# Performance work log

Measured on AMD Instinct MI355X. Metric: run time of the kernel, lower is better.

Reference implementation:

```python
import jax, jax.numpy as jnp
import numpy as np

BN_EPS = 1e-5


def _bn_train(x, gamma, beta):
    # torch BatchNorm1d in training mode: normalize with batch mean and
    # biased batch variance.
    mu = jnp.mean(x, axis=0)
    var = jnp.var(x, axis=0)
    return (x - mu) * jax.lax.rsqrt(var + BN_EPS) * gamma + beta


def setup_inputs() -> dict:
    key = jax.random.key(0)
    ks = jax.random.split(key, 12)
    N, F_D, F_C, E, VOCAB, H = 16384, 26, 10, 16, 200000, 400
    D_IN = (F_D + F_C) * E  # 576
    return {
        "Xi_dense": jax.random.normal(ks[0], (N, F_D, 1), jnp.float32),
        "Xv": jax.random.uniform(ks[1], (N, F_D + F_C), jnp.float32),
        "Wd": jax.random.normal(ks[2], (F_D, E), jnp.float32) * 0.1,
        "bd": jax.random.normal(ks[3], (F_D, E), jnp.float32) * 0.1,
        "tables": jax.random.normal(ks[4], (F_C, VOCAB, E), jnp.float32) * 0.1,
        "W1": jax.random.normal(ks[5], (H, D_IN), jnp.float32) * 0.05,
        "b1": jax.random.normal(ks[6], (H,), jnp.float32) * 0.05,
        "g1": jnp.ones((H,), jnp.float32),
        "be1": jnp.zeros((H,), jnp.float32),
        "W2": jax.random.normal(ks[7], (H, H), jnp.float32) * 0.05,
        "b2": jax.random.normal(ks[8], (H,), jnp.float32) * 0.05,
        "g2": jnp.ones((H,), jnp.float32),
        "be2": jnp.zeros((H,), jnp.float32),
        "bias_vec": jax.random.normal(ks[9], (N,), jnp.float32),
        "Xi_cat": jax.random.randint(ks[10], (N, F_C, 1), 0, VOCAB, jnp.int32),
    }


def reference(Xi_dense, Xv, Wd, bd, tables, W1, b1, g1, be1,
              W2, b2, g2, be2, bias_vec, Xi_cat):
    N = Xi_dense.shape[0]
    # dense fields: per-field Linear(1, E) -> x * W + b, shape (N, 26, E)
    dense_emb = Xi_dense * Wd[None] + bd[None]  # (N,26,1)*(1,26,E) broadcast
    # categorical fields: per-field embedding lookup, shape (N, 10, E)
    cat_emb = jax.vmap(lambda tbl, idx: tbl[idx], in_axes=(0, 1), out_axes=1)(
        tables, Xi_cat[:, :, 0])
    # scale each field embedding by its Xv value
    all_emb = jnp.concatenate([dense_emb, cat_emb], axis=1) * Xv[:, :, None]  # (N,36,E)

    # fm first order: concat of all scaled field embeddings
    fm_first = all_emb.reshape(N, -1)  # (N, 576)
    # fm second order: 0.5 * ((sum)^2 - sum of squares)
    s = jnp.sum(all_emb, axis=1)                       # (N, E)
    fm_second = 0.5 * (s * s - jnp.sum(all_emb * all_emb, axis=1))  # (N, E)

    # deep part: Linear -> BatchNorm (train-mode stats) per hidden layer;
    # dropout p=0 -> identity.
    deep = fm_first
    deep = _bn_train(deep @ W1.T + b1, g1, be1)
    deep = _bn_train(deep @ W2.T + b2, g2, be2)

    total = (jnp.sum(fm_first, axis=1) + jnp.sum(fm_second, axis=1)
             + jnp.sum(deep, axis=1) + bias_vec)
    return total
```

## Files before the change

### kernel.cpp

```cpp
#include <hip/hip_runtime.h>

#define BN_EPS 1e-5f

typedef unsigned short u16;
typedef __attribute__((ext_vector_type(8))) short bf16x8;
typedef __attribute__((ext_vector_type(4))) float f32x4;

__device__ __forceinline__ u16 f2bf(float x) {
  union { float f; unsigned int u; } v; v.f = x;
  unsigned int r = v.u + 0x7fffu + ((v.u >> 16) & 1u);
  return (u16)(r >> 16);
}
__device__ __forceinline__ float bf2f(u16 h) {
  union { unsigned int u; float f; } v; v.u = ((unsigned int)h) << 16;
  return v.f;
}

__device__ __forceinline__ float wave_reduce_sum(float v) {
#pragma unroll
  for (int off = 1; off < 64; off <<= 1) v += __shfl_xor(v, off, 64);
  return v;
}

__device__ __forceinline__ void gload_lds16(const void* g, void* l) {
  __builtin_amdgcn_global_load_lds(
      (const __attribute__((address_space(1))) void*)g,
      (__attribute__((address_space(3))) void*)l, 16, 0, 0);
}

#define NBE 4096
__global__ __launch_bounds__(256) void embed_prep(
    const float* __restrict__ Xi_dense, const float* __restrict__ Xv,
    const float* __restrict__ Wd, const float* __restrict__ bd,
    const float* __restrict__ tables, const int* __restrict__ Xi_cat,
    const float* __restrict__ bias_vec, const float* __restrict__ W1,
    u16* __restrict__ fm_first, float* __restrict__ partial,
    u16* __restrict__ W1h) {
  const int t = threadIdx.x;
  if (blockIdx.x >= NBE) {
    const int base = (blockIdx.x - NBE) * 4096;
#pragma unroll
    for (int e = 0; e < 16; ++e) {
      const int idx = base + e * 256 + t;
      const int r = idx / 576;
      const int j = idx - r * 576;
      W1h[idx] = (r < 400) ? f2bf(W1[r * 576 + j]) : (u16)0;
    }
    return;
  }
  const int lane = t & 63;
  const int n = blockIdx.x * 4 + (t >> 6);

  const float* xv = Xv + n * 36;
  float sum_all = 0.f, s_e = 0.f, q_e = 0.f;

#pragma unroll
  for (int k = 0; k < 9; ++k) {
    const int idx = lane + 64 * k;
    const int f = idx >> 4;
    const int e = idx & 15;
    float val;
    if (f < 26) {
      val = Xi_dense[n * 26 + f] * Wd[f * 16 + e] + bd[f * 16 + e];
    } else {
      const int fc = f - 26;
      const int row = Xi_cat[n * 10 + fc];
      val = tables[(size_t)fc * 200000 * 16 + (size_t)row * 16 + e];
    }
    val *= xv[f];
    fm_first[(size_t)n * 576 + idx] = f2bf(val);
    sum_all += val;
    s_e += val;
    q_e += val * val;
  }

  float s_tot = s_e;
  s_tot += __shfl_xor(s_tot, 16, 64);
  s_tot += __shfl_xor(s_tot, 32, 64);
  float q_tot = q_e;
  q_tot += __shfl_xor(q_tot, 16, 64);
  q_tot += __shfl_xor(q_tot, 32, 64);

  const float fm2 = 0.5f * (s_tot * s_tot - q_tot);
  const float red1 = wave_reduce_sum(sum_all);
  const float red2 = wave_reduce_sum(fm2) * 0.25f;
  if (lane == 0) partial[n] = red1 + red2 + bias_vec[n];
}

__global__ __launch_bounds__(256) void gemm_bf16(
    const u16* __restrict__ A, int lda,
    const u16* __restrict__ W, int ldw,
    const float* __restrict__ bias, int nbias,
    u16* __restrict__ Y, int ldc, int Ncap,
    float* __restrict__ pS, float* __restrict__ pQ, int K) {
  __shared__ u16 As[128 * 32];
  __shared__ u16 Bs[128 * 32];
  __shared__ float rS[2][4][2][16];
  __shared__ float rQ[2][4][2][16];

  const int t = threadIdx.x;
  const int bm = blockIdx.x * 128;
  const int bn = blockIdx.y * 128;
  const int wid = t >> 6, lane = t & 63;
  const int wr = wid >> 1, wc = wid & 1;
  const int lr = lane & 15, lk = (lane >> 4) * 8;
  const int sr = lane >> 2;
  const int sk = (lane & 3) * 8;

  f32x4 acc[4][4] = {};

  for (int kt = 0; kt < K; kt += 32) {
#pragma unroll
    for (int i = 0; i < 2; ++i) {
      const int c = wid * 2 + i;
      gload_lds16(&A[(size_t)(bm + c * 16 + sr) * lda + kt + sk],
                  &As[c * 512]);
      gload_lds16(&W[(size_t)(bn + c * 16 + sr) * ldw + kt + sk],
                  &Bs[c * 512]);
    }
    __syncthreads();

    bf16x8 af[4], bfv[4];
#pragma unroll
    for (int mf = 0; mf < 4; ++mf)
      af[mf] = *(const bf16x8*)&As[(wr * 64 + mf * 16 + lr) * 32 + lk];
#pragma unroll
    for (int nf = 0; nf < 4; ++nf)
      bfv[nf] = *(const bf16x8*)&Bs[(wc * 64 + nf * 16 + lr) * 32 + lk];
#pragma unroll
    for (int mf = 0; mf < 4; ++mf)
#pragma unroll
      for (int nf = 0; nf < 4; ++nf)
        acc[mf][nf] = __builtin_amdgcn_mfma_f32_16x16x32_bf16(
            af[mf], bfv[nf], acc[mf][nf], 0, 0, 0);
    __syncthreads();
  }

  const int l4 = (lane >> 4) * 4;
#pragma unroll
  for (int nf = 0; nf < 4; ++nf) {
    const int col = bn + wc * 64 + nf * 16 + lr;
    const float bb = (col < nbias) ? bias[col] : 0.f;
    float s = 0.f, q = 0.f;
#pragma unroll
    for (int mf = 0; mf < 4; ++mf) {
#pragma unroll
      for (int r = 0; r < 4; ++r) {
        const int row = bm + wr * 64 + mf * 16 + l4 + r;
        const float v = acc[mf][nf][r] + bb;
        s += v;
        q += v * v;
        if (col < Ncap) Y[(size_t)row * ldc + col] = f2bf(v);
      }
    }
    s += __shfl_xor(s, 16, 64);
    s += __shfl_xor(s, 32, 64);
    q += __shfl_xor(q, 16, 64);
    q += __shfl_xor(q, 32, 64);
    if (lane < 16) {
      rS[wc][nf][wr][lr] = s;
      rQ[wc][nf][wr][lr] = q;
    }
  }
  __syncthreads();
  if (t < 128) {
    const int wcc = t >> 6, nff = (t >> 4) & 3, c = t & 15;
    pS[(size_t)(bn + t) * gridDim.x + blockIdx.x] =
        rS[wcc][nff][0][c] + rS[wcc][nff][1][c];
    pQ[(size_t)(bn + t) * gridDim.x + blockIdx.x] =
        rQ[wcc][nff][0][c] + rQ[wcc][nff][1][c];
  }
}

__global__ __launch_bounds__(256) void bn_ac(
    const float* __restrict__ pS, const float* __restrict__ pQ,
    const float* __restrict__ g, const float* __restrict__ be,
    float* __restrict__ a, float* __restrict__ c) {
  const int wid = threadIdx.x >> 6, lane = threadIdx.x & 63;
  const int col = blockIdx.x * 4 + wid;
  float S = pS[(size_t)col * 128 + lane] + pS[(size_t)col * 128 + 64 + lane];
  float Q = pQ[(size_t)col * 128 + lane] + pQ[(size_t)col * 128 + 64 + lane];
#pragma unroll
  for (int off = 1; off < 64; off <<= 1) {
    S += __shfl_xor(S, off, 64);
    Q += __shfl_xor(Q, off, 64);
  }
  if (lane == 0) {
    const float mu = S * (1.f / 16384.f);
    const float var = Q * (1.f / 16384.f) - mu * mu;
    const float aa = g[col] * rsqrtf(var + BN_EPS);
    a[col] = aa;
    c[col] = be[col] - mu * aa;
  }
}

__global__ __launch_bounds__(256) void prep2(
    const float* __restrict__ a1, const float* __restrict__ c1,
    const float* __restrict__ W2, const float* __restrict__ b2,
    u16* __restrict__ W2p, float* __restrict__ b2p) {
  const int t = threadIdx.x;
  const int lane = t & 63;
  const int row = blockIdx.x * 4 + (t >> 6);
  const ushort4 z4 = {0, 0, 0, 0};
  if (row >= 400) {
    const int j1 = lane * 4;
    *(ushort4*)&W2p[(size_t)row * 416 + j1] = z4;
    const int j2 = 256 + lane * 4;
    if (j2 < 416) *(ushort4*)&W2p[(size_t)row * 416 + j2] = z4;
    if (lane == 0) b2p[row] = 0.f;
    return;
  }
  float dot = 0.f;
  {
    const int j = lane * 4;
    const float4 w = *(const float4*)&W2[(size_t)row * 400 + j];
    const float4 la = *(const float4*)&a1[j];
    const float4 lc = *(const float4*)&c1[j];
    ushort4 o = {f2bf(w.x * la.x), f2bf(w.y * la.y), f2bf(w.z * la.z),
                 f2bf(w.w * la.w)};
    *(ushort4*)&W2p[(size_t)row * 416 + j] = o;
    dot += w.x * lc.x + w.y * lc.y + w.z * lc.z + w.w * lc.w;
  }
  {
    const int j = 256 + lane * 4;
    if (j < 400) {
      const float4 w = *(const float4*)&W2[(size_t)row * 400 + j];
      const float4 la = *(const float4*)&a1[j];
      const float4 lc = *(const float4*)&c1[j];
      ushort4 o = {f2bf(w.x * la.x), f2bf(w.y * la.y), f2bf(w.z * la.z),
                   f2bf(w.w * la.w)};
      *(ushort4*)&W2p[(size_t)row * 416 + j] = o;
      dot += w.x * lc.x + w.y * lc.y + w.z * lc.z + w.w * lc.w;
    } else if (j < 416) {
      *(ushort4*)&W2p[(size_t)row * 416 + j] = z4;
    }
  }
  dot = wave_reduce_sum(dot);
  if (lane == 0) b2p[row] = b2[row] + dot;
}

__global__ __launch_bounds__(256) void final_kernel(
    const u16* __restrict__ Y2, const float* __restrict__ a2,
    const float* __restrict__ c2, const float* __restrict__ partial,
    float* __restrict__ out) {
  const int t = threadIdx.x;
  const int lane = t & 63;
  const int wid = t >> 6;
  const int j0 = lane * 8;
  float ar[8], cr[8];
  if (j0 < 400) {
    const float4 a0 = *(const float4*)&a2[j0];
    const float4 a1v = *(const float4*)&a2[j0 + 4];
    const float4 c0 = *(const float4*)&c2[j0];
    const float4 c1v = *(const float4*)&c2[j0 + 4];
    ar[0] = a0.x; ar[1] = a0.y; ar[2] = a0.z; ar[3] = a0.w;
    ar[4] = a1v.x; ar[5] = a1v.y; ar[6] = a1v.z; ar[7] = a1v.w;
    cr[0] = c0.x; cr[1] = c0.y; cr[2] = c0.z; cr[3] = c0.w;
    cr[4] = c1v.x; cr[5] = c1v.y; cr[6] = c1v.z; cr[7] = c1v.w;
  } else {
#pragma unroll
    for (int k = 0; k < 8; ++k) { ar[k] = 0.f; cr[k] = 0.f; }
  }
#pragma unroll
  for (int r = 0; r < 4; ++r) {
    const int n = blockIdx.x * 16 + wid * 4 + r;
    float acc = 0.f;
    if (j0 < 400) {
      const bf16x8 y = *(const bf16x8*)&Y2[(size_t)n * 400 + j0];
#pragma unroll
      for (int k = 0; k < 8; ++k)
        acc += fmaf(ar[k], bf2f((u16)y[k]), cr[k]);
    }
    acc = wave_reduce_sum(acc);
    if (lane == 0) out[n] = partial[n] + acc;
  }
}

extern "C" void kernel_launch(void* const* d_in, const int* in_sizes, int n_in,
                              void* d_out, int out_size, void* d_ws,
                              size_t ws_size, hipStream_t stream) {
  const float* Xi_dense = (const float*)d_in[0];
  const float* Xv = (const float*)d_in[1];
  const float* Wd = (const float*)d_in[2];
  const float* bd = (const float*)d_in[3];
  const float* tables = (const float*)d_in[4];
  const float* W1 = (const float*)d_in[5];
  const float* b1 = (const float*)d_in[6];
  const float* g1 = (const float*)d_in[7];
  const float* be1 = (const float*)d_in[8];
  const float* W2 = (const float*)d_in[9];
  const float* b2 = (const float*)d_in[10];
  const float* g2 = (const float*)d_in[11];
  const float* be2 = (const float*)d_in[12];
  const float* bias_vec = (const float*)d_in[13];
  const int* Xi_cat = (const int*)d_in[14];

  constexpr int N = 16384;
  constexpr int DIN = 576;
  constexpr int H = 400;
  constexpr int KP = 416;
  constexpr int WPAD = 512;
  constexpr int MB = 128;

  u16* fm_first = (u16*)d_ws;
  u16* Y1h = fm_first + (size_t)N * DIN;
  u16* Y2h = Y1h + (size_t)N * KP;
  u16* W1h = Y2h + (size_t)N * H;
  u16* W2p = W1h + (size_t)WPAD * DIN;
  float* fptr = (float*)(W2p + (size_t)WPAD * KP);
  float* partial = fptr;
  float* pS = partial + N;
  float* pQ = pS + WPAD * MB;
  float* a1 = pQ + WPAD * MB;
  float* c1 = a1 + WPAD;
  float* a2 = c1 + WPAD;
  float* c2 = a2 + WPAD;
  float* b2p = c2 + WPAD;

  embed_prep<<<NBE + 72, 256, 0, stream>>>(Xi_dense, Xv, Wd, bd, tables,
                                           Xi_cat, bias_vec, W1, fm_first,
                                           partial, W1h);

  dim3 gg(MB, 4);
  gemm_bf16<<<gg, 256, 0, stream>>>(fm_first, DIN, W1h, DIN, b1, H,
                                    Y1h, KP, KP, pS, pQ, DIN);

  bn_ac<<<100, 256, 0, stream>>>(pS, pQ, g1, be1, a1, c1);
  prep2<<<MB, 256, 0, stream>>>(a1, c1, W2, b2, W2p, b2p);

  gemm_bf16<<<gg, 256, 0, stream>>>(Y1h, KP, W2p, KP, b2p, H,
                                    Y2h, H, H, pS, pQ, KP);

  bn_ac<<<100, 256, 0, stream>>>(pS, pQ, g2, be2, a2, c2);

  final_kernel<<<N / 16, 256, 0, stream>>>(Y2h, a2, c2, partial,
                                           (float*)d_out);
}
```

Measured before the change: 71.13 us.

## Shrink GEMM M-tile to 64, trim padded N-tile, and swizzle block order

The GEMM moves from 128x128 to 64x128 tiles and launches 1024 blocks on a 1D grid instead of 512. The last N-tile, which covers columns 384-511 with only 16 of them useful for H=400, now uses a 2-fragment variant in which half the waves stay idle and skip the padded MFMA work. Block indices are remapped with a stride-8 swizzle to change how tiles are assigned across CUs/XCDs. This raises occupancy and trims wasted padded compute, at the cost of more A-tile reloads and more partial BN sums that bn_ac has to reduce.

```diff
diff --git a/kernel.cpp b/kernel.cpp
--- a/kernel.cpp
+++ b/kernel.cpp
@@ -87,99 +87,125 @@
   if (lane == 0) partial[n] = red1 + red2 + bias_vec[n];
 }
 
+template <int NFR>
+__device__ __forceinline__ void gemm_body(
+    const u16* __restrict__ A, int lda, const u16* __restrict__ W, int ldw,
+    const float* __restrict__ bias, int nbias, u16* __restrict__ Y, int ldc,
+    int Ncap, float* __restrict__ pS, float* __restrict__ pQ, int K, int nxb,
+    int bx, int by, u16* As, u16* Bs, float (&rS)[2][4][2][16],
+    float (&rQ)[2][4][2][16]) {
+  const int t = threadIdx.x;
+  const int bm = bx * 64;
+  const int bn = by * 128;
+  const int wid = t >> 6, lane = t & 63;
+  const int wr = wid >> 1, wc = wid & 1;
+  const int lr = lane & 15, lk = (lane >> 4) * 8;
+  const int sr = lane >> 2;
+  const int sk = (lane & 3) * 8;
+  const bool active = (NFR == 4) || (wc == 0);
+
+  f32x4 acc[2][NFR] = {};
+
+  for (int kt = 0; kt < K; kt += 32) {
+    gload_lds16(&A[(size_t)(bm + wid * 16 + sr) * lda + kt + sk],
+                &As[wid * 512]);
+#pragma unroll
+    for (int i = 0; i < 2; ++i) {
+      const int c = wid * 2 + i;
+      if (NFR == 4 || c < 2)
+        gload_lds16(&W[(size_t)(bn + c * 16 + sr) * ldw + kt + sk],
+                    &Bs[c * 512]);
+    }
+    __syncthreads();
+
+    if (active) {
+      bf16x8 af[2], bfv[NFR];
+#pragma unroll
+      for (int mf = 0; mf < 2; ++mf)
+        af[mf] = *(const bf16x8*)&As[(wr * 32 + mf * 16 + lr) * 32 + lk];
+#pragma unroll
+      for (int nf = 0; nf < NFR; ++nf)
+        bfv[nf] = *(const bf16x8*)&Bs[(wc * 64 + nf * 16 + lr) * 32 + lk];
+#pragma unroll
+      for (int mf = 0; mf < 2; ++mf)
+#pragma unroll
+        for (int nf = 0; nf < NFR; ++nf)
+          acc[mf][nf] = __builtin_amdgcn_mfma_f32_16x16x32_bf16(
+              af[mf], bfv[nf], acc[mf][nf], 0, 0, 0);
+    }
+    __syncthreads();
+  }
+
+  const int l4 = (lane >> 4) * 4;
+  if (active) {
+#pragma unroll
+    for (int nf = 0; nf < NFR; ++nf) {
+      const int col = bn + wc * 64 + nf * 16 + lr;
+      const float bb = (col < nbias) ? bias[col] : 0.f;
+      float s = 0.f, q = 0.f;
+#pragma unroll
+      for (int mf = 0; mf < 2; ++mf) {
+#pragma unroll
+        for (int r = 0; r < 4; ++r) {
+          const int row = bm + wr * 32 + mf * 16 + l4 + r;
+          const float v = acc[mf][nf][r] + bb;
+          s += v;
+          q += v * v;
+          if (col < Ncap) Y[(size_t)row * ldc + col] = f2bf(v);
+        }
+      }
+      s += __shfl_xor(s, 16, 64);
+      s += __shfl_xor(s, 32, 64);
+      q += __shfl_xor(q, 16, 64);
+      q += __shfl_xor(q, 32, 64);
+      if (lane < 16) {
+        rS[wc][nf][wr][lr] = s;
+        rQ[wc][nf][wr][lr] = q;
+      }
+    }
+  }
+  __syncthreads();
+  if (t < (NFR == 4 ? 128 : 32)) {
+    const int wcc = t >> 6, nff = (t >> 4) & 3, c = t & 15;
+    pS[(size_t)(bn + t) * nxb + bx] =
+        rS[wcc][nff][0][c] + rS[wcc][nff][1][c];
+    pQ[(size_t)(bn + t) * nxb + bx] =
+        rQ[wcc][nff][0][c] + rQ[wcc][nff][1][c];
+  }
+}
+
 __global__ __launch_bounds__(256) void gemm_bf16(
     const u16* __restrict__ A, int lda,
     const u16* __restrict__ W, int ldw,
     const float* __restrict__ bias, int nbias,
     u16* __restrict__ Y, int ldc, int Ncap,
-    float* __restrict__ pS, float* __restrict__ pQ, int K) {
-  __shared__ u16 As[128 * 32];
+    float* __restrict__ pS, float* __restrict__ pQ, int K, int nxb) {
+  __shared__ u16 As[64 * 32];
   __shared__ u16 Bs[128 * 32];
   __shared__ float rS[2][4][2][16];
   __shared__ float rQ[2][4][2][16];
-
-  const int t = threadIdx.x;
-  const int bm = blockIdx.x * 128;
-  const int bn = blockIdx.y * 128;
-  const int wid = t >> 6, lane = t & 63;
-  const int wr = wid >> 1, wc = wid & 1;
-  const int lr = lane & 15, lk = (lane >> 4) * 8;
-  const int sr = lane >> 2;
-  const int sk = (lane & 3) * 8;
-
-  f32x4 acc[4][4] = {};
-
-  for (int kt = 0; kt < K; kt += 32) {
-#pragma unroll
-    for (int i = 0; i < 2; ++i) {
-      const int c = wid * 2 + i;
-      gload_lds16(&A[(size_t)(bm + c * 16 + sr) * lda + kt + sk],
-                  &As[c * 512]);
-      gload_lds16(&W[(size_t)(bn + c * 16 + sr) * ldw + kt + sk],
-                  &Bs[c * 512]);
-    }
-    __syncthreads();
-
-    bf16x8 af[4], bfv[4];
-#pragma unroll
-    for (int mf = 0; mf < 4; ++mf)
-      af[mf] = *(const bf16x8*)&As[(wr * 64 + mf * 16 + lr) * 32 + lk];
-#pragma unroll
-    for (int nf = 0; nf < 4; ++nf)
-      bfv[nf] = *(const bf16x8*)&Bs[(wc * 64 + nf * 16 + lr) * 32 + lk];
-#pragma unroll
-    for (int mf = 0; mf < 4; ++mf)
-#pragma unroll
-      for (int nf = 0; nf < 4; ++nf)
-        acc[mf][nf] = __builtin_amdgcn_mfma_f32_16x16x32_bf16(
-            af[mf], bfv[nf], acc[mf][nf], 0, 0, 0);
-    __syncthreads();
-  }
-
-  const int l4 = (lane >> 4) * 4;
-#pragma unroll
-  for (int nf = 0; nf < 4; ++nf) {
-    const int col = bn + wc * 64 + nf * 16 + lr;
-    const float bb = (col < nbias) ? bias[col] : 0.f;
-    float s = 0.f, q = 0.f;
-#pragma unroll
-    for (int mf = 0; mf < 4; ++mf) {
-#pragma unroll
-      for (int r = 0; r < 4; ++r) {
-        const int row = bm + wr * 64 + mf * 16 + l4 + r;
-        const float v = acc[mf][nf][r] + bb;
-        s += v;
-        q += v * v;
-        if (col < Ncap) Y[(size_t)row * ldc + col] = f2bf(v);
-      }
-    }
-    s += __shfl_xor(s, 16, 64);
-    s += __shfl_xor(s, 32, 64);
-    q += __shfl_xor(q, 16, 64);
-    q += __shfl_xor(q, 32, 64);
-    if (lane < 16) {
-      rS[wc][nf][wr][lr] = s;
-      rQ[wc][nf][wr][lr] = q;
-    }
-  }
-  __syncthreads();
-  if (t < 128) {
-    const int wcc = t >> 6, nff = (t >> 4) & 3, c = t & 15;
-    pS[(size_t)(bn + t) * gridDim.x + blockIdx.x] =
-        rS[wcc][nff][0][c] + rS[wcc][nff][1][c];
-    pQ[(size_t)(bn + t) * gridDim.x + blockIdx.x] =
-        rQ[wcc][nff][0][c] + rQ[wcc][nff][1][c];
-  }
+  const int bid = blockIdx.x;
+  const int l = (bid & 7) * (gridDim.x >> 3) + (bid >> 3);
+  const int bx = l >> 2, by = l & 3;
+  if (by < 3)
+    gemm_body<4>(A, lda, W, ldw, bias, nbias, Y, ldc, Ncap, pS, pQ, K, nxb,
+                 bx, by, As, Bs, rS, rQ);
+  else
+    gemm_body<2>(A, lda, W, ldw, bias, nbias, Y, ldc, Ncap, pS, pQ, K, nxb,
+                 bx, by, As, Bs, rS, rQ);
 }
 
 __global__ __launch_bounds__(256) void bn_ac(
     const float* __restrict__ pS, const float* __restrict__ pQ,
     const float* __restrict__ g, const float* __restrict__ be,
-    float* __restrict__ a, float* __restrict__ c) {
+    float* __restrict__ a, float* __restrict__ c, int nxb) {
   const int wid = threadIdx.x >> 6, lane = threadIdx.x & 63;
   const int col = blockIdx.x * 4 + wid;
-  float S = pS[(size_t)col * 128 + lane] + pS[(size_t)col * 128 + 64 + lane];
-  float Q = pQ[(size_t)col * 128 + lane] + pQ[(size_t)col * 128 + 64 + lane];
+  float S = 0.f, Q = 0.f;
+  for (int i = lane; i < nxb; i += 64) {
+    S += pS[(size_t)col * nxb + i];
+    Q += pQ[(size_t)col * nxb + i];
+  }
 #pragma unroll
   for (int off = 1; off < 64; off <<= 1) {
     S += __shfl_xor(S, off, 64);
@@ -300,7 +326,7 @@
   constexpr int H = 400;
   constexpr int KP = 416;
   constexpr int WPAD = 512;
-  constexpr int MB = 128;
+  constexpr int NXB = 256;
 
   u16* fm_first = (u16*)d_ws;
   u16* Y1h = fm_first + (size_t)N * DIN;
@@ -310,8 +336,8 @@
   float* fptr = (float*)(W2p + (size_t)WPAD * KP);
   float* partial = fptr;
   float* pS = partial + N;
-  float* pQ = pS + WPAD * MB;
-  float* a1 = pQ + WPAD * MB;
+  float* pQ = pS + WPAD * NXB;
+  float* a1 = pQ + WPAD * NXB;
   float* c1 = a1 + WPAD;
   float* a2 = c1 + WPAD;
   float* c2 = a2 + WPAD;
@@ -321,17 +347,16 @@
                                            Xi_cat, bias_vec, W1, fm_first,
                                            partial, W1h);
 
-  dim3 gg(MB, 4);
-  gemm_bf16<<<gg, 256, 0, stream>>>(fm_first, DIN, W1h, DIN, b1, H,
-                                    Y1h, KP, KP, pS, pQ, DIN);
-
-  bn_ac<<<100, 256, 0, stream>>>(pS, pQ, g1, be1, a1, c1);
-  prep2<<<MB, 256, 0, stream>>>(a1, c1, W2, b2, W2p, b2p);
-
-  gemm_bf16<<<gg, 256, 0, stream>>>(Y1h, KP, W2p, KP, b2p, H,
-                                    Y2h, H, H, pS, pQ, KP);
-
-  bn_ac<<<100, 256, 0, stream>>>(pS, pQ, g2, be2, a2, c2);
+  gemm_bf16<<<NXB * 4, 256, 0, stream>>>(fm_first, DIN, W1h, DIN, b1, H,
+                                         Y1h, KP, KP, pS, pQ, DIN, NXB);
+
+  bn_ac<<<100, 256, 0, stream>>>(pS, pQ, g1, be1, a1, c1, NXB);
+  prep2<<<128, 256, 0, stream>>>(a1, c1, W2, b2, W2p, b2p);
+
+  gemm_bf16<<<NXB * 4, 256, 0, stream>>>(Y1h, KP, W2p, KP, b2p, H,
+                                         Y2h, H, H, pS, pQ, KP, NXB);
+
+  bn_ac<<<100, 256, 0, stream>>>(pS, pQ, g2, be2, a2, c2, NXB);
 
   final_kernel<<<N / 16, 256, 0, stream>>>(Y2h, a2, c2, partial,
                                            (float*)d_out);
```

Result: faster. 67.88 us (-4.6%).

## Keep full weight panel in LDS and stream A from global into registers

Applied to the files above, without the earlier changes.

Replaces the 128x128 LDS-tiled GEMM with a templated 256x64-tile kernel. It loads the block's whole 64-column weight panel (padded) into LDS once. Each wave then streams its 64 A rows straight from global memory into registers, prefetching two k-steps ahead, so the per-k-step barriers go away. A swizzled 1D grid of 448 blocks and MFMA priority hints are added, and the BN partial-stat reduction is adapted to 64 row-blocks. This trades large LDS use and uncoalesced direct A loads for removing synchronization and improving B reuse.

```diff
diff --git a/kernel.cpp b/kernel.cpp
--- a/kernel.cpp
+++ b/kernel.cpp
@@ -20,12 +20,6 @@
 #pragma unroll
   for (int off = 1; off < 64; off <<= 1) v += __shfl_xor(v, off, 64);
   return v;
-}
-
-__device__ __forceinline__ void gload_lds16(const void* g, void* l) {
-  __builtin_amdgcn_global_load_lds(
-      (const __attribute__((address_space(1))) void*)g,
-      (__attribute__((address_space(3))) void*)l, 16, 0, 0);
 }
 
 #define NBE 4096
@@ -87,66 +81,91 @@
   if (lane == 0) partial[n] = red1 + red2 + bias_vec[n];
 }
 
-__global__ __launch_bounds__(256) void gemm_bf16(
-    const u16* __restrict__ A, int lda,
-    const u16* __restrict__ W, int ldw,
+template <int K>
+__global__ __launch_bounds__(256) void gemm_bres(
+    const u16* __restrict__ A,
+    const u16* __restrict__ W,
     const float* __restrict__ bias, int nbias,
     u16* __restrict__ Y, int ldc, int Ncap,
-    float* __restrict__ pS, float* __restrict__ pQ, int K) {
-  __shared__ u16 As[128 * 32];
-  __shared__ u16 Bs[128 * 32];
-  __shared__ float rS[2][4][2][16];
-  __shared__ float rQ[2][4][2][16];
+    float* __restrict__ pS, float* __restrict__ pQ) {
+  constexpr int NI = K / 32;
+  constexpr int PADK = K + 8;
+  constexpr int CPR = K / 8;
+  __shared__ u16 Bs[64 * PADK];
+  __shared__ float rS[4][64];
+  __shared__ float rQ[4][64];
 
   const int t = threadIdx.x;
-  const int bm = blockIdx.x * 128;
-  const int bn = blockIdx.y * 128;
+  const int bid = blockIdx.x;
+  const int l = (bid & 7) * 56 + (bid >> 3);
+  const int bx = l / 7;
+  const int by = l - bx * 7;
+  const int bm = bx * 256, bn = by * 64;
+
+  for (int chunk = t; chunk < 64 * CPR; chunk += 256) {
+    const int r = chunk / CPR;
+    const int cc = (chunk - r * CPR) * 8;
+    *(bf16x8*)&Bs[r * PADK + cc] =
+        *(const bf16x8*)&W[(size_t)(bn + r) * K + cc];
+  }
+  __syncthreads();
+
   const int wid = t >> 6, lane = t & 63;
-  const int wr = wid >> 1, wc = wid & 1;
   const int lr = lane & 15, lk = (lane >> 4) * 8;
-  const int sr = lane >> 2;
-  const int sk = (lane & 3) * 8;
+  const int rowb = bm + wid * 64;
+
+  const u16* Ap = A + (size_t)(rowb + lr) * K + lk;
 
   f32x4 acc[4][4] = {};
-
-  for (int kt = 0; kt < K; kt += 32) {
-#pragma unroll
-    for (int i = 0; i < 2; ++i) {
-      const int c = wid * 2 + i;
-      gload_lds16(&A[(size_t)(bm + c * 16 + sr) * lda + kt + sk],
-                  &As[c * 512]);
-      gload_lds16(&W[(size_t)(bn + c * 16 + sr) * ldw + kt + sk],
-                  &Bs[c * 512]);
-    }
-    __syncthreads();
-
-    bf16x8 af[4], bfv[4];
-#pragma unroll
-    for (int mf = 0; mf < 4; ++mf)
-      af[mf] = *(const bf16x8*)&As[(wr * 64 + mf * 16 + lr) * 32 + lk];
+  bf16x8 afA[4], afB[4];
+#pragma unroll
+  for (int mf = 0; mf < 4; ++mf) {
+    afA[mf] = *(const bf16x8*)&Ap[(size_t)mf * 16 * K];
+    afB[mf] = *(const bf16x8*)&Ap[(size_t)mf * 16 * K + 32];
+  }
+
+#pragma unroll
+  for (int i = 0; i < NI; ++i) {
+    const int kt = i * 32;
+    bf16x8 bv[4];
 #pragma unroll
     for (int nf = 0; nf < 4; ++nf)
-      bfv[nf] = *(const bf16x8*)&Bs[(wc * 64 + nf * 16 + lr) * 32 + lk];
+      bv[nf] = *(const bf16x8*)&Bs[(nf * 16 + lr) * PADK + kt + lk];
+    bf16x8 afN[4];
+    if (i + 2 < NI) {
+#pragma unroll
+      for (int mf = 0; mf < 4; ++mf)
+        afN[mf] = *(const bf16x8*)&Ap[(size_t)mf * 16 * K + kt + 64];
+    } else {
+#pragma unroll
+      for (int mf = 0; mf < 4; ++mf) afN[mf] = afB[mf];
+    }
+    __builtin_amdgcn_s_setprio(1);
 #pragma unroll
     for (int mf = 0; mf < 4; ++mf)
 #pragma unroll
       for (int nf = 0; nf < 4; ++nf)
         acc[mf][nf] = __builtin_amdgcn_mfma_f32_16x16x32_bf16(
-            af[mf], bfv[nf], acc[mf][nf], 0, 0, 0);
-    __syncthreads();
+            afA[mf], bv[nf], acc[mf][nf], 0, 0, 0);
+    __builtin_amdgcn_s_setprio(0);
+#pragma unroll
+    for (int mf = 0; mf < 4; ++mf) {
+      afA[mf] = afB[mf];
+      afB[mf] = afN[mf];
+    }
   }
 
   const int l4 = (lane >> 4) * 4;
 #pragma unroll
   for (int nf = 0; nf < 4; ++nf) {
-    const int col = bn + wc * 64 + nf * 16 + lr;
+    const int col = bn + nf * 16 + lr;
     const float bb = (col < nbias) ? bias[col] : 0.f;
     float s = 0.f, q = 0.f;
 #pragma unroll
     for (int mf = 0; mf < 4; ++mf) {
 #pragma unroll
       for (int r = 0; r < 4; ++r) {
-        const int row = bm + wr * 64 + mf * 16 + l4 + r;
+        const int row = rowb + mf * 16 + l4 + r;
         const float v = acc[mf][nf][r] + bb;
         s += v;
         q += v * v;
@@ -158,28 +177,30 @@
     q += __shfl_xor(q, 16, 64);
     q += __shfl_xor(q, 32, 64);
     if (lane < 16) {
-      rS[wc][nf][wr][lr] = s;
-      rQ[wc][nf][wr][lr] = q;
+      rS[wid][nf * 16 + lr] = s;
+      rQ[wid][nf * 16 + lr] = q;
     }
   }
   __syncthreads();
-  if (t < 128) {
-    const int wcc = t >> 6, nff = (t >> 4) & 3, c = t & 15;
-    pS[(size_t)(bn + t) * gridDim.x + blockIdx.x] =
-        rS[wcc][nff][0][c] + rS[wcc][nff][1][c];
-    pQ[(size_t)(bn + t) * gridDim.x + blockIdx.x] =
-        rQ[wcc][nff][0][c] + rQ[wcc][nff][1][c];
+  if (t < 64) {
+    const float S = rS[0][t] + rS[1][t] + rS[2][t] + rS[3][t];
+    const float Q = rQ[0][t] + rQ[1][t] + rQ[2][t] + rQ[3][t];
+    pS[(size_t)(bn + t) * 64 + bx] = S;
+    pQ[(size_t)(bn + t) * 64 + bx] = Q;
   }
 }
 
 __global__ __launch_bounds__(256) void bn_ac(
     const float* __restrict__ pS, const float* __restrict__ pQ,
     const float* __restrict__ g, const float* __restrict__ be,
-    float* __restrict__ a, float* __restrict__ c) {
+    float* __restrict__ a, float* __restrict__ c, int nxb) {
   const int wid = threadIdx.x >> 6, lane = threadIdx.x & 63;
   const int col = blockIdx.x * 4 + wid;
-  float S = pS[(size_t)col * 128 + lane] + pS[(size_t)col * 128 + 64 + lane];
-  float Q = pQ[(size_t)col * 128 + lane] + pQ[(size_t)col * 128 + 64 + lane];
+  float S = 0.f, Q = 0.f;
+  for (int i = lane; i < nxb; i += 64) {
+    S += pS[(size_t)col * nxb + i];
+    Q += pQ[(size_t)col * nxb + i];
+  }
 #pragma unroll
   for (int off = 1; off < 64; off <<= 1) {
     S += __shfl_xor(S, off, 64);
@@ -300,7 +321,7 @@
   constexpr int H = 400;
   constexpr int KP = 416;
   constexpr int WPAD = 512;
-  constexpr int MB = 128;
+  constexpr int NXB = 64;
 
   u16* fm_first = (u16*)d_ws;
   u16* Y1h = fm_first + (size_t)N * DIN;
@@ -310,8 +331,8 @@
   float* fptr = (float*)(W2p + (size_t)WPAD * KP);
   float* partial = fptr;
   float* pS = partial + N;
-  float* pQ = pS + WPAD * MB;
-  float* a1 = pQ + WPAD * MB;
+  float* pQ = pS + WPAD * NXB;
+  float* a1 = pQ + WPAD * NXB;
   float* c1 = a1 + WPAD;
   float* a2 = c1 + WPAD;
   float* c2 = a2 + WPAD;
@@ -321,17 +342,16 @@
                                            Xi_cat, bias_vec, W1, fm_first,
                                            partial, W1h);
 
-  dim3 gg(MB, 4);
-  gemm_bf16<<<gg, 256, 0, stream>>>(fm_first, DIN, W1h, DIN, b1, H,
-                                    Y1h, KP, KP, pS, pQ, DIN);
-
-  bn_ac<<<100, 256, 0, stream>>>(pS, pQ, g1, be1, a1, c1);
-  prep2<<<MB, 256, 0, stream>>>(a1, c1, W2, b2, W2p, b2p);
-
-  gemm_bf16<<<gg, 256, 0, stream>>>(Y1h, KP, W2p, KP, b2p, H,
-                                    Y2h, H, H, pS, pQ, KP);
-
-  bn_ac<<<100, 256, 0, stream>>>(pS, pQ, g2, be2, a2, c2);
+  gemm_bres<DIN><<<NXB * 7, 256, 0, stream>>>(fm_first, W1h, b1, H,
+                                              Y1h, KP, KP, pS, pQ);
+
+  bn_ac<<<100, 256, 0, stream>>>(pS, pQ, g1, be1, a1, c1, NXB);
+  prep2<<<128, 256, 0, stream>>>(a1, c1, W2, b2, W2p, b2p);
+
+  gemm_bres<KP><<<NXB * 7, 256, 0, stream>>>(Y1h, W2p, b2p, H,
+                                             Y2h, H, H, pS, pQ);
+
+  bn_ac<<<100, 256, 0, stream>>>(pS, pQ, g2, be2, a2, c2, NXB);
 
   final_kernel<<<N / 16, 256, 0, stream>>>(Y2h, a2, c2, partial,
                                            (float*)d_out);
```

After: 77.51 us. +9.0%, slower.
